# Optimization experiments

Measured on AMD Instinct MI355X. Metric: run time of the kernel, lower is better.

## Reference

```python
import jax, jax.numpy as jnp
import numpy as np

K = 16
H = 128

def _gelu(x):
    return jax.nn.gelu(x, approximate=False)  # torch nn.GELU default (erf)

def _knn_idx(xyz, k):
    # squared pairwise distances; topk of squared dist == topk of cdist (monotone)
    sq = jnp.sum(xyz * xyz, axis=-1)  # [B,N]
    d2 = sq[:, :, None] + sq[:, None, :] - 2.0 * jnp.einsum('bnd,bmd->bnm', xyz, xyz)
    n = xyz.shape[1]
    d2 = d2.at[:, jnp.arange(n), jnp.arange(n)].set(-1.0)  # force self first
    _, idx = jax.lax.top_k(-d2, min(k + 1, n))  # smallest distances
    return idx[..., 1:]  # drop self -> [B,N,K]

def _gather(feat, idx):
    # feat [B,N,C], idx [B,N,K] -> [B,N,K,C]
    return jax.vmap(lambda f, i: f[i])(feat, idx)

def setup_inputs() -> dict:
    key = jax.random.key(0)
    ks = jax.random.split(key, 13)
    s = 0.05
    return {
        'points': jax.random.normal(ks[0], (4, 4096, 6), jnp.float32),
        'Wc1': jax.random.normal(ks[1], (3, H), jnp.float32) * s,
        'bc1': jnp.zeros((H,), jnp.float32),
        'Wc2': jax.random.normal(ks[2], (H, H), jnp.float32) * s,
        'bc2': jnp.zeros((H,), jnp.float32),
        'Wn1': jax.random.normal(ks[3], (4, H), jnp.float32) * s,
        'bn1': jnp.zeros((H,), jnp.float32),
        'Wn2': jax.random.normal(ks[4], (H, H), jnp.float32) * s,
        'bn2': jnp.zeros((H,), jnp.float32),
        'Wo1': jax.random.normal(ks[5], (2 * H, H), jnp.float32) * s,
        'bo1': jnp.zeros((H,), jnp.float32),
        'Wo2': jax.random.normal(ks[6], (H, H), jnp.float32) * s,
        'bo2': jnp.zeros((H,), jnp.float32),
        'k': K,
    }

def reference(points, Wc1, bc1, Wc2, bc2, Wn1, bn1, Wn2, bn2, Wo1, bo1, Wo2, bo2, k):
    xyz = points[..., :3]
    normals = points[..., 3:6]
    idx = jax.lax.stop_gradient(_knn_idx(xyz, k))  # [B,N,K]

    # coord branch: relative neighbor coords -> MLP -> max over K
    rel_xyz = _gather(xyz, idx) - xyz[:, :, None, :]          # [B,N,K,3]
    h = _gelu(rel_xyz @ Wc1 + bc1) @ Wc2 + bc2                # [B,N,K,H]
    coord_feat = jnp.max(h, axis=2)                           # [B,N,H]

    # normal branch: neighbor normals + 1 - cos variation
    neigh_n = _gather(normals, idx)                           # [B,N,K,3]
    variation = 1.0 - jnp.sum(normals[:, :, None, :] * neigh_n, axis=-1, keepdims=True)
    nin = jnp.concatenate([neigh_n, variation], axis=-1)      # [B,N,K,4]
    g = _gelu(nin @ Wn1 + bn1) @ Wn2 + bn2                    # [B,N,K,H]
    normal_feat = jnp.max(g, axis=2)                          # [B,N,H]

    cat = jnp.concatenate([coord_feat, normal_feat], axis=-1) # [B,N,2H]
    return _gelu(cat @ Wo1 + bo1) @ Wo2 + bo2                 # [B,N,H]
```

## Files before the change

### kernel.cpp

```cpp
#include <hip/hip_runtime.h>
#include <math.h>

#define BATCH 4
#define NPTS 4096
#define KNBR 16
#define HDIM 128

typedef __attribute__((ext_vector_type(8))) short bf16x8;
typedef __attribute__((ext_vector_type(4))) float f32x4;
typedef unsigned long long u64;

#define WSOFF_W (1u << 20)
#define WC_HI 0
#define WC_LO 16384
#define WN_HI 32768
#define WN_LO 49152
#define WO1_HI 65536
#define WO1_LO 98304
#define WO2_HI 131072
#define WO2_LO 147456

__device__ __forceinline__ float gelu_f(float x) {
    const float z = x * 0.7071067811865476f;
    const float u = fabsf(z);
    const float z2 = z * z;
    const float t = __builtin_amdgcn_rcpf(fmaf(0.3275911f, u, 1.0f));
    const float E = __expf(-z2);
    float p = fmaf(t, 1.061405429f, -1.453152027f);
    p = fmaf(t, p, 1.421413741f);
    p = fmaf(t, p, -0.284496736f);
    p = fmaf(t, p, 0.254829592f);
    p = p * t;
    const float e = fmaf(-p, E, 1.0f);
    const float hx = 0.5f * x;
    return fmaf(fabsf(hx), e, hx);
}

__device__ __forceinline__ void bsplit(float x, short& hi, short& lo) {
    const unsigned u = __float_as_uint(x);
    hi = (short)(u >> 16);
    const float r = x - __uint_as_float(u & 0xffff0000u);
    lo = (short)(__float_as_uint(r) >> 16);
}

__device__ __forceinline__ u64 umin64(u64 a, u64 b) { return a < b ? a : b; }
__device__ __forceinline__ u64 umax64(u64 a, u64 b) { return a > b ? a : b; }

__device__ __forceinline__ u64 readlane_u64(u64 v, int src) {
    const unsigned lo = (unsigned)__builtin_amdgcn_readlane((int)(unsigned)v, src);
    const unsigned hi = (unsigned)__builtin_amdgcn_readlane((int)(unsigned)(v >> 32), src);
    return ((u64)hi << 32) | lo;
}

__global__ __launch_bounds__(256) void prep_points(const float* __restrict__ pts,
                                                   float4* __restrict__ ctab) {
    const int e = blockIdx.x * 256 + threadIdx.x;
    const float* __restrict__ p = pts + (size_t)e * 6;
    const float x = p[0], y = p[1], z = p[2];
    const float sq = x * x + y * y + z * z;
    ctab[e] = make_float4(x, y, z, sq);
}

__global__ __launch_bounds__(256) void prep_weights(
    const float* __restrict__ Wc2, const float* __restrict__ Wn2,
    const float* __restrict__ Wo1, const float* __restrict__ Wo2,
    unsigned short* __restrict__ wbuf)
{
    const int e = blockIdx.x * 256 + threadIdx.x;
    const float* src;
    unsigned short *dh, *dl;
    int idx;
    if (e < 16384)      { src = Wc2; dh = wbuf + WC_HI;  dl = wbuf + WC_LO;  idx = e; }
    else if (e < 32768) { src = Wn2; dh = wbuf + WN_HI;  dl = wbuf + WN_LO;  idx = e - 16384; }
    else if (e < 65536) { src = Wo1; dh = wbuf + WO1_HI; dl = wbuf + WO1_LO; idx = e - 32768; }
    else                { src = Wo2; dh = wbuf + WO2_HI; dl = wbuf + WO2_LO; idx = e - 65536; }
    const int j = idx & 7;
    const int l = (idx >> 3) & 63;
    const int tile = idx >> 9;
    const int ct = tile & 7;
    const int ks = tile >> 3;
    const int n = (l & 15) + 16 * ct;
    const int k = ks * 32 + ((l >> 4) << 3) + j;
    const float x = src[k * 128 + n];
    short hi, lo;
    bsplit(x, hi, lo);
    dh[idx] = (unsigned short)hi;
    dl[idx] = (unsigned short)lo;
}

__global__ __launch_bounds__(256) void knn_kernel(const float4* __restrict__ ctab,
                                                  int* __restrict__ idx_out) {
    const int wq = blockIdx.x * 4 + (threadIdx.x >> 6);
    const int n0 = (wq * 2) & (NPTS - 1);
    const int n1 = n0 + 1;
    const int b = (wq * 2) >> 12;
    const int lane = threadIdx.x & 63;
    const float4* __restrict__ cb = ctab + (size_t)b * NPTS;

    const float4 q0 = cb[n0];
    const float4 q1 = cb[n1];

    u64 v0, v1;
    {
        const int m = lane;
        const float4 cc = cb[m];
        const float d0 = q0.x * cc.x + q0.y * cc.y + q0.z * cc.z;
        const float d1 = q1.x * cc.x + q1.y * cc.y + q1.z * cc.z;
        const float e0 = fmaxf((q0.w + cc.w) - 2.0f * d0, 0.0f);
        const float e1 = fmaxf((q1.w + cc.w) - 2.0f * d1, 0.0f);
        v0 = ((u64)__float_as_uint(e0) << 32) | (unsigned)m;
        v1 = ((u64)__float_as_uint(e1) << 32) | (unsigned)m;
        if (m == n0) v0 = ~0ull;
        if (m == n1) v1 = ~0ull;
#pragma unroll
        for (int k = 2; k <= 64; k <<= 1) {
#pragma unroll
            for (int j = k >> 1; j > 0; j >>= 1) {
                const u64 p0 = __shfl_xor(v0, j, 64);
                const u64 p1 = __shfl_xor(v1, j, 64);
                const bool keepmin = (((lane & j) == 0) == ((lane & k) == 0));
                v0 = keepmin ? umin64(v0, p0) : umax64(v0, p0);
                v1 = keepmin ? umin64(v1, p1) : umax64(v1, p1);
            }
        }
    }
    const u64 t1 = __shfl(v1, lane & 15, 64);
    u64 run = (lane < 16) ? v0 : ((lane < 32) ? t1 : ~0ull);
    u64 max0 = readlane_u64(run, 15);
    u64 max1 = readlane_u64(run, 31);

    for (int c = 1; c < NPTS / 64; ++c) {
        const int m = lane + 64 * c;
        const float4 cc = cb[m];
        const float d0 = q0.x * cc.x + q0.y * cc.y + q0.z * cc.z;
        const float d1 = q1.x * cc.x + q1.y * cc.y + q1.z * cc.z;
        float e0 = fmaxf((q0.w + cc.w) - 2.0f * d0, 0.0f);
        float e1 = fmaxf((q1.w + cc.w) - 2.0f * d1, 0.0f);
        u64 key0 = ((u64)__float_as_uint(e0) << 32) | (unsigned)m;
        u64 key1 = ((u64)__float_as_uint(e1) << 32) | (unsigned)m;
        if (m == n0) key0 = ~0ull;
        if (m == n1) key1 = ~0ull;

        u64 mask0 = __ballot(key0 < max0);
        while (mask0) {
            const int src = (int)__builtin_ctzll(mask0);
            const u64 K = readlane_u64(key0, src);
            u64 prev = __shfl_up(run, 1, 64);
            if ((lane & 15) == 0) prev = 0;
            const u64 cand = (run < K) ? run : ((prev < K) ? K : prev);
            if ((lane >> 4) == 0) run = cand;
            max0 = readlane_u64(run, 15);
            mask0 &= mask0 - 1;
            mask0 &= __ballot(key0 < max0);
        }
        u64 mask1 = __ballot(key1 < max1);
        while (mask1) {
            const int src = (int)__builtin_ctzll(mask1);
            const u64 K = readlane_u64(key1, src);
            u64 prev = __shfl_up(run, 1, 64);
            if ((lane & 15) == 0) prev = 0;
            const u64 cand = (run < K) ? run : ((prev < K) ? K : prev);
            if ((lane >> 4) == 1) run = cand;
            max1 = readlane_u64(run, 31);
            mask1 &= mask1 - 1;
            mask1 &= __ballot(key1 < max1);
        }
    }

    if (lane < KNBR)
        idx_out[((size_t)b * NPTS + n0) * KNBR + lane] = (int)(run & 0xffffffffull);
    else if (lane < 2 * KNBR)
        idx_out[((size_t)b * NPTS + n1) * KNBR + (lane - KNBR)] = (int)(run & 0xffffffffull);
}

template<int NIN>
__device__ __forceinline__ void branch_compute(
    const float (* __restrict__ inp)[4],
    const float* __restrict__ w1s,
    const float* __restrict__ b1s,
    const float* __restrict__ b2s,
    const unsigned short* __restrict__ w2hi,
    const unsigned short* __restrict__ w2lo,
    unsigned short (* __restrict__ catH)[264],
    unsigned short (* __restrict__ catL)[264],
    int colbase, int w, int l)
{
    const int lr = l & 15;
    const int lq = l >> 4;
    const int kb = lq * 8;

    f32x4 acc[2][8];
#pragma unroll
    for (int rt = 0; rt < 2; ++rt)
#pragma unroll
        for (int ct = 0; ct < 8; ++ct)
            acc[rt][ct] = (f32x4){0.f, 0.f, 0.f, 0.f};

    for (int ks = 0; ks < 4; ++ks) {
        const int c0 = ks * 32 + kb;
        float wr[NIN][8], bb[8];
#pragma unroll
        for (int d = 0; d < NIN; ++d) {
            *(float4*)&wr[d][0] = *(const float4*)(w1s + (d << 7) + c0);
            *(float4*)&wr[d][4] = *(const float4*)(w1s + (d << 7) + c0 + 4);
        }
        *(float4*)&bb[0] = *(const float4*)(b1s + c0);
        *(float4*)&bb[4] = *(const float4*)(b1s + c0 + 4);

        bf16x8 ah[2], al[2];
#pragma unroll
        for (int rt = 0; rt < 2; ++rt) {
            const int row = 32 * w + 16 * rt + lr;
            const float4 rv = *(const float4*)&inp[row][0];
#pragma unroll
            for (int jj = 0; jj < 8; ++jj) {
                float x = bb[jj] + rv.x * wr[0][jj] + rv.y * wr[1][jj] + rv.z * wr[2][jj];
                if (NIN == 4) x += rv.w * wr[3][jj];
                x = gelu_f(x);
                short hi, lo;
                bsplit(x, hi, lo);
                ah[rt][jj] = hi;
                al[rt][jj] = lo;
            }
        }
#pragma unroll
        for (int ct = 0; ct < 8; ++ct) {
            const size_t off = ((size_t)((ks * 8 + ct) * 64 + l)) * 8;
            const bf16x8 bh = *(const bf16x8*)(w2hi + off);
            const bf16x8 bl = *(const bf16x8*)(w2lo + off);
#pragma unroll
            for (int rt = 0; rt < 2; ++rt) {
                acc[rt][ct] = __builtin_amdgcn_mfma_f32_16x16x32_bf16(ah[rt], bh, acc[rt][ct], 0, 0, 0);
                acc[rt][ct] = __builtin_amdgcn_mfma_f32_16x16x32_bf16(ah[rt], bl, acc[rt][ct], 0, 0, 0);
                acc[rt][ct] = __builtin_amdgcn_mfma_f32_16x16x32_bf16(al[rt], bh, acc[rt][ct], 0, 0, 0);
            }
        }
    }
#pragma unroll
    for (int rt = 0; rt < 2; ++rt) {
        const int p = 2 * w + rt;
#pragma unroll
        for (int ct = 0; ct < 8; ++ct) {
            const f32x4 a = acc[rt][ct];
            float m = fmaxf(fmaxf(a[0], a[1]), fmaxf(a[2], a[3]));
            m = fmaxf(m, __shfl_xor(m, 16));
            m = fmaxf(m, __shfl_xor(m, 32));
            const int col = lr + 16 * ct;
            const float v = m + b2s[col];
            if (lq == 0) {
                short hi, lo;
                bsplit(v, hi, lo);
                catH[p][colbase + col] = (unsigned short)hi;
                catL[p][colbase + col] = (unsigned short)lo;
            }
        }
    }
}

__global__ __launch_bounds__(256, 3) void mlp_mfma(
    const float* __restrict__ pts, const int* __restrict__ knn_idx,
    const float* __restrict__ Wc1, const float* __restrict__ bc1,
    const float* __restrict__ bc2,
    const float* __restrict__ Wn1, const float* __restrict__ bn1,
    const float* __restrict__ bn2,
    const float* __restrict__ bo1, const float* __restrict__ bo2,
    const unsigned short* __restrict__ wbuf,
    float* __restrict__ outp)
{
    __shared__ __align__(16) float rel[128][4];
    __shared__ __align__(16) float nin[128][4];
    __shared__ float qpt[8][6];
    __shared__ __align__(16) unsigned short catH[8][264];
    __shared__ __align__(16) unsigned short catL[8][264];
    __shared__ __align__(16) unsigned short o1H[8][136];
    __shared__ __align__(16) unsigned short o1L[8][136];
    __shared__ __align__(16) float w1c[3 * 128];
    __shared__ __align__(16) float w1n[4 * 128];
    __shared__ __align__(16) float b1c[128], b2c[128], b1n[128], b2n[128], bo1s[128], bo2s[128];

    const int t = threadIdx.x;
    const int w = t >> 6;
    const int l = t & 63;
    const int lr = l & 15;
    const int lq = l >> 4;
    const int kb = lq * 8;
    const int blk = blockIdx.x;
    const int b = blk >> 9;
    const int n0 = (blk & 511) * 8;
    const float* __restrict__ base = pts + (size_t)b * NPTS * 6;

    for (int i = t; i < 384; i += 256) w1c[i] = Wc1[i];
    for (int i = t; i < 512; i += 256) w1n[i] = Wn1[i];
    if (t < 128) {
        b1c[t] = bc1[t]; b2c[t] = bc2[t];
        b1n[t] = bn1[t]; b2n[t] = bn2[t];
        bo1s[t] = bo1[t]; bo2s[t] = bo2[t];
    }
    if (t < 48) qpt[t / 6][t % 6] = base[(size_t)(n0 + t / 6) * 6 + (t % 6)];
    __syncthreads();
    if (t < 128) {
        const int p = t >> 4;
        const int m = knn_idx[((size_t)b * NPTS + n0 + p) * KNBR + (t & 15)];
        const float cx = base[(size_t)m * 6 + 0];
        const float cy = base[(size_t)m * 6 + 1];
        const float cz = base[(size_t)m * 6 + 2];
        const float nx = base[(size_t)m * 6 + 3];
        const float ny = base[(size_t)m * 6 + 4];
        const float nz = base[(size_t)m * 6 + 5];
        rel[t][0] = cx - qpt[p][0];
        rel[t][1] = cy - qpt[p][1];
        rel[t][2] = cz - qpt[p][2];
        rel[t][3] = 0.0f;
        nin[t][0] = nx; nin[t][1] = ny; nin[t][2] = nz;
        nin[t][3] = 1.0f - (qpt[p][3] * nx + qpt[p][4] * ny + qpt[p][5] * nz);
    }
    __syncthreads();

    branch_compute<3>(rel, w1c, b1c, b2c, wbuf + WC_HI, wbuf + WC_LO,
                      catH, catL, 0, w, l);
    branch_compute<4>(nin, w1n, b1n, b2n, wbuf + WN_HI, wbuf + WN_LO,
                      catH, catL, 128, w, l);
    __syncthreads();

    {
        f32x4 a1[2];
        a1[0] = (f32x4){0.f, 0.f, 0.f, 0.f};
        a1[1] = (f32x4){0.f, 0.f, 0.f, 0.f};
#pragma unroll
        for (int ks = 0; ks < 8; ++ks) {
            const int c0 = ks * 32 + kb;
            const bf16x8 ah = *(const bf16x8*)&catH[lr & 7][c0];
            const bf16x8 al = *(const bf16x8*)&catL[lr & 7][c0];
#pragma unroll
            for (int c2 = 0; c2 < 2; ++c2) {
                const int ct = 2 * w + c2;
                const unsigned short* wp = wbuf + WO1_HI + ((size_t)((ks * 8 + ct) * 64 + l)) * 8;
                const bf16x8 bh = *(const bf16x8*)wp;
                const bf16x8 bl = *(const bf16x8*)(wp + (WO1_LO - WO1_HI));
                a1[c2] = __builtin_amdgcn_mfma_f32_16x16x32_bf16(ah, bh, a1[c2], 0, 0, 0);
                a1[c2] = __builtin_amdgcn_mfma_f32_16x16x32_bf16(ah, bl, a1[c2], 0, 0, 0);
                a1[c2] = __builtin_amdgcn_mfma_f32_16x16x32_bf16(al, bh, a1[c2], 0, 0, 0);
            }
        }
#pragma unroll
        for (int c2 = 0; c2 < 2; ++c2) {
            const int col = lr + 16 * (2 * w + c2);
            const float bo = bo1s[col];
#pragma unroll
            for (int r = 0; r < 4; ++r) {
                const int prow = lq * 4 + r;
                if (prow < 8) {
                    const float x = gelu_f(a1[c2][r] + bo);
                    short hi, lo;
                    bsplit(x, hi, lo);
                    o1H[prow][col] = (unsigned short)hi;
                    o1L[prow][col] = (unsigned short)lo;
                }
            }
        }
    }
    __syncthreads();
    {
        f32x4 a2[2];
        a2[0] = (f32x4){0.f, 0.f, 0.f, 0.f};
        a2[1] = (f32x4){0.f, 0.f, 0.f, 0.f};
#pragma unroll
        for (int ks = 0; ks < 4; ++ks) {
            const int c0 = ks * 32 + kb;
            const bf16x8 ah = *(const bf16x8*)&o1H[lr & 7][c0];
            const bf16x8 al = *(const bf16x8*)&o1L[lr & 7][c0];
#pragma unroll
            for (int c2 = 0; c2 < 2; ++c2) {
                const int ct = 2 * w + c2;
                const unsigned short* wp = wbuf + WO2_HI + ((size_t)((ks * 8 + ct) * 64 + l)) * 8;
                const bf16x8 bh = *(const bf16x8*)wp;
                const bf16x8 bl = *(const bf16x8*)(wp + (WO2_LO - WO2_HI));
                a2[c2] = __builtin_amdgcn_mfma_f32_16x16x32_bf16(ah, bh, a2[c2], 0, 0, 0);
                a2[c2] = __builtin_amdgcn_mfma_f32_16x16x32_bf16(ah, bl, a2[c2], 0, 0, 0);
                a2[c2] = __builtin_amdgcn_mfma_f32_16x16x32_bf16(al, bh, a2[c2], 0, 0, 0);
            }
        }
#pragma unroll
        for (int c2 = 0; c2 < 2; ++c2) {
            const int col = lr + 16 * (2 * w + c2);
            const float bo = bo2s[col];
#pragma unroll
            for (int r = 0; r < 4; ++r) {
                const int prow = lq * 4 + r;
                if (prow < 8)
                    outp[((size_t)b * NPTS + n0 + prow) * HDIM + col] = a2[c2][r] + bo;
            }
        }
    }
}

extern "C" void kernel_launch(void* const* d_in, const int* in_sizes, int n_in,
                              void* d_out, int out_size, void* d_ws, size_t ws_size,
                              hipStream_t stream) {
    const float* pts = (const float*)d_in[0];
    const float* Wc1 = (const float*)d_in[1];
    const float* bc1 = (const float*)d_in[2];
    const float* Wc2 = (const float*)d_in[3];
    const float* bc2 = (const float*)d_in[4];
    const float* Wn1 = (const float*)d_in[5];
    const float* bn1 = (const float*)d_in[6];
    const float* Wn2 = (const float*)d_in[7];
    const float* bn2 = (const float*)d_in[8];
    const float* Wo1 = (const float*)d_in[9];
    const float* bo1 = (const float*)d_in[10];
    const float* Wo2 = (const float*)d_in[11];
    const float* bo2 = (const float*)d_in[12];
    float* outp = (float*)d_out;
    int* idx = (int*)d_ws;
    float4* ctab = (float4*)((char*)d_ws + WSOFF_W);
    unsigned short* wbuf = (unsigned short*)((char*)d_ws + WSOFF_W);

    prep_points<<<dim3(BATCH * NPTS / 256), dim3(256), 0, stream>>>(pts, ctab);
    knn_kernel<<<dim3(BATCH * NPTS / 8), dim3(256), 0, stream>>>(ctab, idx);
    prep_weights<<<dim3(320), dim3(256), 0, stream>>>(Wc2, Wn2, Wo1, Wo2, wbuf);
    mlp_mfma<<<dim3(BATCH * NPTS / 8), dim3(256), 0, stream>>>(
        pts, idx, Wc1, bc1, bc2, Wn1, bn1, bn2, bo1, bo2, wbuf, outp);
}
```

Measured before the change: 168.7 us.

## Use 8 waves per MLP block, one point per wave

The MLP kernel moves from 256 to 512 threads per block. Each of the 8 waves now handles one point's 16 neighbors in the branch stage and one 16-column tile in the output layers, where before 4 waves each handled two points and two column tiles. This halves accumulator registers per wave and raises wave-level parallelism, aiming to hide latency better. The cost is more redundant weight loads from global memory per block, since every wave streams the full W2 panels for the branches.

```diff
diff --git a/kernel.cpp b/kernel.cpp
--- a/kernel.cpp
+++ b/kernel.cpp
@@ -189,12 +189,10 @@
     const int lq = l >> 4;
     const int kb = lq * 8;
 
-    f32x4 acc[2][8];
-#pragma unroll
-    for (int rt = 0; rt < 2; ++rt)
-#pragma unroll
-        for (int ct = 0; ct < 8; ++ct)
-            acc[rt][ct] = (f32x4){0.f, 0.f, 0.f, 0.f};
+    f32x4 acc[8];
+#pragma unroll
+    for (int ct = 0; ct < 8; ++ct)
+        acc[ct] = (f32x4){0.f, 0.f, 0.f, 0.f};
 
     for (int ks = 0; ks < 4; ++ks) {
         const int c0 = ks * 32 + kb;
@@ -207,57 +205,47 @@
         *(float4*)&bb[0] = *(const float4*)(b1s + c0);
         *(float4*)&bb[4] = *(const float4*)(b1s + c0 + 4);
 
-        bf16x8 ah[2], al[2];
-#pragma unroll
-        for (int rt = 0; rt < 2; ++rt) {
-            const int row = 32 * w + 16 * rt + lr;
-            const float4 rv = *(const float4*)&inp[row][0];
-#pragma unroll
-            for (int jj = 0; jj < 8; ++jj) {
-                float x = bb[jj] + rv.x * wr[0][jj] + rv.y * wr[1][jj] + rv.z * wr[2][jj];
-                if (NIN == 4) x += rv.w * wr[3][jj];
-                x = gelu_f(x);
-                short hi, lo;
-                bsplit(x, hi, lo);
-                ah[rt][jj] = hi;
-                al[rt][jj] = lo;
-            }
+        const int row = 16 * w + lr;
+        const float4 rv = *(const float4*)&inp[row][0];
+        bf16x8 ah, al;
+#pragma unroll
+        for (int jj = 0; jj < 8; ++jj) {
+            float x = bb[jj] + rv.x * wr[0][jj] + rv.y * wr[1][jj] + rv.z * wr[2][jj];
+            if (NIN == 4) x += rv.w * wr[3][jj];
+            x = gelu_f(x);
+            short hi, lo;
+            bsplit(x, hi, lo);
+            ah[jj] = hi;
+            al[jj] = lo;
         }
 #pragma unroll
         for (int ct = 0; ct < 8; ++ct) {
             const size_t off = ((size_t)((ks * 8 + ct) * 64 + l)) * 8;
             const bf16x8 bh = *(const bf16x8*)(w2hi + off);
             const bf16x8 bl = *(const bf16x8*)(w2lo + off);
-#pragma unroll
-            for (int rt = 0; rt < 2; ++rt) {
-                acc[rt][ct] = __builtin_amdgcn_mfma_f32_16x16x32_bf16(ah[rt], bh, acc[rt][ct], 0, 0, 0);
-                acc[rt][ct] = __builtin_amdgcn_mfma_f32_16x16x32_bf16(ah[rt], bl, acc[rt][ct], 0, 0, 0);
-                acc[rt][ct] = __builtin_amdgcn_mfma_f32_16x16x32_bf16(al[rt], bh, acc[rt][ct], 0, 0, 0);
-            }
-        }
-    }
-#pragma unroll
-    for (int rt = 0; rt < 2; ++rt) {
-        const int p = 2 * w + rt;
-#pragma unroll
-        for (int ct = 0; ct < 8; ++ct) {
-            const f32x4 a = acc[rt][ct];
-            float m = fmaxf(fmaxf(a[0], a[1]), fmaxf(a[2], a[3]));
-            m = fmaxf(m, __shfl_xor(m, 16));
-            m = fmaxf(m, __shfl_xor(m, 32));
-            const int col = lr + 16 * ct;
-            const float v = m + b2s[col];
-            if (lq == 0) {
-                short hi, lo;
-                bsplit(v, hi, lo);
-                catH[p][colbase + col] = (unsigned short)hi;
-                catL[p][colbase + col] = (unsigned short)lo;
-            }
-        }
-    }
-}
-
-__global__ __launch_bounds__(256, 3) void mlp_mfma(
+            acc[ct] = __builtin_amdgcn_mfma_f32_16x16x32_bf16(ah, bh, acc[ct], 0, 0, 0);
+            acc[ct] = __builtin_amdgcn_mfma_f32_16x16x32_bf16(ah, bl, acc[ct], 0, 0, 0);
+            acc[ct] = __builtin_amdgcn_mfma_f32_16x16x32_bf16(al, bh, acc[ct], 0, 0, 0);
+        }
+    }
+#pragma unroll
+    for (int ct = 0; ct < 8; ++ct) {
+        const f32x4 a = acc[ct];
+        float m = fmaxf(fmaxf(a[0], a[1]), fmaxf(a[2], a[3]));
+        m = fmaxf(m, __shfl_xor(m, 16));
+        m = fmaxf(m, __shfl_xor(m, 32));
+        const int col = lr + 16 * ct;
+        const float v = m + b2s[col];
+        if (lq == 0) {
+            short hi, lo;
+            bsplit(v, hi, lo);
+            catH[w][colbase + col] = (unsigned short)hi;
+            catL[w][colbase + col] = (unsigned short)lo;
+        }
+    }
+}
+
+__global__ __launch_bounds__(512, 4) void mlp_mfma(
     const float* __restrict__ pts, const int* __restrict__ knn_idx,
     const float* __restrict__ Wc1, const float* __restrict__ bc1,
     const float* __restrict__ bc2,
@@ -289,8 +277,8 @@
     const int n0 = (blk & 511) * 8;
     const float* __restrict__ base = pts + (size_t)b * NPTS * 6;
 
-    for (int i = t; i < 384; i += 256) w1c[i] = Wc1[i];
-    for (int i = t; i < 512; i += 256) w1n[i] = Wn1[i];
+    if (t < 384) w1c[t] = Wc1[t];
+    w1n[t] = Wn1[t];
     if (t < 128) {
         b1c[t] = bc1[t]; b2c[t] = bc2[t];
         b1n[t] = bn1[t]; b2n[t] = bn2[t];
@@ -323,73 +311,55 @@
     __syncthreads();
 
     {
-        f32x4 a1[2];
-        a1[0] = (f32x4){0.f, 0.f, 0.f, 0.f};
-        a1[1] = (f32x4){0.f, 0.f, 0.f, 0.f};
+        f32x4 a1 = (f32x4){0.f, 0.f, 0.f, 0.f};
 #pragma unroll
         for (int ks = 0; ks < 8; ++ks) {
             const int c0 = ks * 32 + kb;
             const bf16x8 ah = *(const bf16x8*)&catH[lr & 7][c0];
             const bf16x8 al = *(const bf16x8*)&catL[lr & 7][c0];
-#pragma unroll
-            for (int c2 = 0; c2 < 2; ++c2) {
-                const int ct = 2 * w + c2;
-                const unsigned short* wp = wbuf + WO1_HI + ((size_t)((ks * 8 + ct) * 64 + l)) * 8;
-                const bf16x8 bh = *(const bf16x8*)wp;
-                const bf16x8 bl = *(const bf16x8*)(wp + (WO1_LO - WO1_HI));
-                a1[c2] = __builtin_amdgcn_mfma_f32_16x16x32_bf16(ah, bh, a1[c2], 0, 0, 0);
-                a1[c2] = __builtin_amdgcn_mfma_f32_16x16x32_bf16(ah, bl, a1[c2], 0, 0, 0);
-                a1[c2] = __builtin_amdgcn_mfma_f32_16x16x32_bf16(al, bh, a1[c2], 0, 0, 0);
-            }
-        }
-#pragma unroll
-        for (int c2 = 0; c2 < 2; ++c2) {
-            const int col = lr + 16 * (2 * w + c2);
-            const float bo = bo1s[col];
-#pragma unroll
-            for (int r = 0; r < 4; ++r) {
-                const int prow = lq * 4 + r;
-                if (prow < 8) {
-                    const float x = gelu_f(a1[c2][r] + bo);
-                    short hi, lo;
-                    bsplit(x, hi, lo);
-                    o1H[prow][col] = (unsigned short)hi;
-                    o1L[prow][col] = (unsigned short)lo;
-                }
+            const unsigned short* wp = wbuf + WO1_HI + ((size_t)((ks * 8 + w) * 64 + l)) * 8;
+            const bf16x8 bh = *(const bf16x8*)wp;
+            const bf16x8 bl = *(const bf16x8*)(wp + (WO1_LO - WO1_HI));
+            a1 = __builtin_amdgcn_mfma_f32_16x16x32_bf16(ah, bh, a1, 0, 0, 0);
+            a1 = __builtin_amdgcn_mfma_f32_16x16x32_bf16(ah, bl, a1, 0, 0, 0);
+            a1 = __builtin_amdgcn_mfma_f32_16x16x32_bf16(al, bh, a1, 0, 0, 0);
+        }
+        const int col = lr + 16 * w;
+        const float bo = bo1s[col];
+#pragma unroll
+        for (int r = 0; r < 4; ++r) {
+            const int prow = lq * 4 + r;
+            if (prow < 8) {
+                const float x = gelu_f(a1[r] + bo);
+                short hi, lo;
+                bsplit(x, hi, lo);
+                o1H[prow][col] = (unsigned short)hi;
+                o1L[prow][col] = (unsigned short)lo;
             }
         }
     }
     __syncthreads();
     {
-        f32x4 a2[2];
-        a2[0] = (f32x4){0.f, 0.f, 0.f, 0.f};
-        a2[1] = (f32x4){0.f, 0.f, 0.f, 0.f};
+        f32x4 a2 = (f32x4){0.f, 0.f, 0.f, 0.f};
 #pragma unroll
         for (int ks = 0; ks < 4; ++ks) {
             const int c0 = ks * 32 + kb;
             const bf16x8 ah = *(const bf16x8*)&o1H[lr & 7][c0];
             const bf16x8 al = *(const bf16x8*)&o1L[lr & 7][c0];
-#pragma unroll
-            for (int c2 = 0; c2 < 2; ++c2) {
-                const int ct = 2 * w + c2;
-                const unsigned short* wp = wbuf + WO2_HI + ((size_t)((ks * 8 + ct) * 64 + l)) * 8;
-                const bf16x8 bh = *(const bf16x8*)wp;
-                const bf16x8 bl = *(const bf16x8*)(wp + (WO2_LO - WO2_HI));
-                a2[c2] = __builtin_amdgcn_mfma_f32_16x16x32_bf16(ah, bh, a2[c2], 0, 0, 0);
-                a2[c2] = __builtin_amdgcn_mfma_f32_16x16x32_bf16(ah, bl, a2[c2], 0, 0, 0);
-                a2[c2] = __builtin_amdgcn_mfma_f32_16x16x32_bf16(al, bh, a2[c2], 0, 0, 0);
-            }
-        }
-#pragma unroll
-        for (int c2 = 0; c2 < 2; ++c2) {
-            const int col = lr + 16 * (2 * w + c2);
-            const float bo = bo2s[col];
-#pragma unroll
-            for (int r = 0; r < 4; ++r) {
-                const int prow = lq * 4 + r;
-                if (prow < 8)
-                    outp[((size_t)b * NPTS + n0 + prow) * HDIM + col] = a2[c2][r] + bo;
-            }
+            const unsigned short* wp = wbuf + WO2_HI + ((size_t)((ks * 8 + w) * 64 + l)) * 8;
+            const bf16x8 bh = *(const bf16x8*)wp;
+            const bf16x8 bl = *(const bf16x8*)(wp + (WO2_LO - WO2_HI));
+            a2 = __builtin_amdgcn_mfma_f32_16x16x32_bf16(ah, bh, a2, 0, 0, 0);
+            a2 = __builtin_amdgcn_mfma_f32_16x16x32_bf16(ah, bl, a2, 0, 0, 0);
+            a2 = __builtin_amdgcn_mfma_f32_16x16x32_bf16(al, bh, a2, 0, 0, 0);
+        }
+        const int col = lr + 16 * w;
+        const float bo = bo2s[col];
+#pragma unroll
+        for (int r = 0; r < 4; ++r) {
+            const int prow = lq * 4 + r;
+            if (prow < 8)
+                outp[((size_t)b * NPTS + n0 + prow) * HDIM + col] = a2[r] + bo;
         }
     }
 }
@@ -418,6 +388,6 @@
     prep_points<<<dim3(BATCH * NPTS / 256), dim3(256), 0, stream>>>(pts, ctab);
     knn_kernel<<<dim3(BATCH * NPTS / 8), dim3(256), 0, stream>>>(ctab, idx);
     prep_weights<<<dim3(320), dim3(256), 0, stream>>>(Wc2, Wn2, Wo1, Wo2, wbuf);
-    mlp_mfma<<<dim3(BATCH * NPTS / 8), dim3(256), 0, stream>>>(
+    mlp_mfma<<<dim3(BATCH * NPTS / 8), dim3(512), 0, stream>>>(
         pts, idx, Wc1, bc1, bc2, Wn1, bn1, bn2, bo1, bo2, wbuf, outp);
 }
```

After: 180.3 us. +6.9%, slower.
